# Kernel tuning notes

Measured on AMD Instinct MI355X. Metric: run time of the kernel, lower is better.

Reference implementation:

```python
import jax, jax.numpy as jnp
import numpy as np

N = 50000      # nodes
E = 800000     # directed edges (before self-loops)
IN = 128       # in_channels
H = 4          # heads (layers 1,2)
C = 64         # hidden_channels per head
OUT = 512      # out_channels of final Linear
LEAKY_SLOPE = 0.2


def _gat_layer(x, src, dst, n, W, a_src, a_dst, b, concat):
    """PyG GATConv (v1): shared linear, additive attention, segment softmax over dst."""
    heads, ch = a_src.shape
    xl = (x @ W).reshape(n, heads, ch)                       # [N,H,C]
    as_n = jnp.sum(xl * a_src, axis=-1)                      # [N,H] alpha_src per node
    ad_n = jnp.sum(xl * a_dst, axis=-1)                      # [N,H] alpha_dst per node
    logits = jax.nn.leaky_relu(as_n[src] + ad_n[dst], LEAKY_SLOPE)  # [Etot,H]
    m = jax.lax.stop_gradient(jax.ops.segment_max(logits, dst, num_segments=n))
    p = jnp.exp(logits - m[dst])
    denom = jax.ops.segment_sum(p, dst, num_segments=n) + 1e-16
    alpha = p / denom[dst]                                   # segment softmax over incoming edges
    out = jax.ops.segment_sum(xl[src] * alpha[:, :, None], dst, num_segments=n)  # [N,H,C]
    out = out.reshape(n, heads * ch) if concat else out.mean(axis=1)
    return out + b


def setup_inputs() -> dict:
    key = jax.random.key(0)
    ks = jax.random.split(key, 16)

    def gl(k, shape, fan_in):
        return jax.random.normal(k, shape, dtype=jnp.float32) * np.float32(1.0 / np.sqrt(fan_in))

    x = jax.random.normal(ks[0], (N, IN), dtype=jnp.float32)
    edge_index = jax.random.randint(ks[1], (2, E), 0, N, dtype=jnp.int32)

    inp = {
        "x": x,
        "edge_index": edge_index,
        # layer 1: in -> H*C (concat)
        "W1": gl(ks[2], (IN, H * C), IN),
        "a_src1": gl(ks[3], (H, C), C),
        "a_dst1": gl(ks[4], (H, C), C),
        "b1": jnp.zeros((H * C,), jnp.float32),
        # layer 2: H*C -> H*C (concat)
        "W2": gl(ks[5], (H * C, H * C), H * C),
        "a_src2": gl(ks[6], (H, C), C),
        "a_dst2": gl(ks[7], (H, C), C),
        "b2": jnp.zeros((H * C,), jnp.float32),
        # layer 3: H*C -> C (1 head, no concat)
        "W3": gl(ks[8], (H * C, C), H * C),
        "a_src3": gl(ks[9], (1, C), C),
        "a_dst3": gl(ks[10], (1, C), C),
        "b3": jnp.zeros((C,), jnp.float32),
        # final fc: C -> OUT
        "Wfc": gl(ks[11], (C, OUT), C),
        "bfc": jnp.zeros((OUT,), jnp.float32),
    }
    return inp


def reference(x, edge_index, W1, a_src1, a_dst1, b1, W2, a_src2, a_dst2, b2,
              W3, a_src3, a_dst3, b3, Wfc, bfc):
    n = x.shape[0]
    loop = jnp.arange(n, dtype=edge_index.dtype)             # PyG GATConv adds self-loops
    src = jnp.concatenate([edge_index[0], loop])
    dst = jnp.concatenate([edge_index[1], loop])

    h = jax.nn.relu(_gat_layer(x, src, dst, n, W1, a_src1, a_dst1, b1, True))
    h = jax.nn.relu(_gat_layer(h, src, dst, n, W2, a_src2, a_dst2, b2, True))
    h = jax.nn.relu(_gat_layer(h, src, dst, n, W3, a_src3, a_dst3, b3, False))
    return jax.nn.relu(h @ Wfc + bfc)                        # [N, OUT]
```

## Files before the change

kernel.cpp:

```cpp
#include <hip/hip_runtime.h>
#include <cstdint>
#include <cstddef>

typedef unsigned short ushort_t;
typedef __bf16 bf16x8 __attribute__((ext_vector_type(8)));
typedef float f32x4 __attribute__((ext_vector_type(4)));

__device__ __forceinline__ float b2f(ushort_t u) {
    return __uint_as_float(((unsigned int)u) << 16);
}
__device__ __forceinline__ ushort_t f2b(float f) {
    __bf16 h = (__bf16)f;
    return *(ushort_t*)&h;
}

__device__ __forceinline__ void stage8(const float* __restrict__ g, ushort_t* s) {
    float4 f0 = *(const float4*)g;
    float4 f1 = *(const float4*)(g + 4);
    union { ushort_t u[8]; uint4 v; } t;
    t.u[0] = f2b(f0.x); t.u[1] = f2b(f0.y); t.u[2] = f2b(f0.z); t.u[3] = f2b(f0.w);
    t.u[4] = f2b(f1.x); t.u[5] = f2b(f1.y); t.u[6] = f2b(f1.z); t.u[7] = f2b(f1.w);
    *(uint4*)s = t.v;
}
__device__ __forceinline__ void stage8(const ushort_t* __restrict__ g, ushort_t* s) {
    *(float4*)s = *(const float4*)g;
}

__global__ __launch_bounds__(256) void transpose_kernel(const float* __restrict__ W,
                                                        ushort_t* __restrict__ WT,
                                                        int K, int N2) {
    int id = blockIdx.x * 256 + threadIdx.x;
    if (id >= K * N2) return;
    int n = id / K, k = id - n * K;
    WT[id] = f2b(W[k * N2 + n]);
}

__global__ __launch_bounds__(256) void degree_kernel(const int* __restrict__ ei_dst,
                                                     int* __restrict__ deg, int E, int Etot) {
    int e = blockIdx.x * 256 + threadIdx.x;
    if (e >= Etot) return;
    int d = (e < E) ? ei_dst[e] : (e - E);
    atomicAdd(&deg[d], 1);
}

__global__ __launch_bounds__(1024) void scan_kernel(const int* __restrict__ deg,
                                                    int* __restrict__ rowoff, int n) {
    __shared__ int sums[1024];
    int t = threadIdx.x;
    int chunk = (n + 1023) >> 10;
    int start = t * chunk;
    int end = min(start + chunk, n);
    int s = 0;
    for (int i = start; i < end; i++) s += deg[i];
    sums[t] = s;
    __syncthreads();
    for (int off = 1; off < 1024; off <<= 1) {
        int v = (t >= off) ? sums[t - off] : 0;
        __syncthreads();
        sums[t] += v;
        __syncthreads();
    }
    int base = (t == 0) ? 0 : sums[t - 1];
    for (int i = start; i < end; i++) { rowoff[i] = base; base += deg[i]; }
    if (t == 1023) rowoff[n] = sums[1023];
}

__global__ __launch_bounds__(256) void scatter_kernel(const int* __restrict__ ei_src,
                                                      const int* __restrict__ ei_dst,
                                                      const int* __restrict__ rowoff,
                                                      int* __restrict__ cursor,
                                                      int* __restrict__ ssrc, int E, int Etot) {
    int e = blockIdx.x * 256 + threadIdx.x;
    if (e >= Etot) return;
    int s, d;
    if (e < E) { s = ei_src[e]; d = ei_dst[e]; } else { s = d = e - E; }
    int pos = rowoff[d] + atomicAdd(&cursor[d], 1);
    ssrc[pos] = s;
}

template <typename TA, bool EPI>
__global__ __launch_bounds__(256) void gemm_mfma(const TA* __restrict__ A,
                                                 const ushort_t* __restrict__ WT,
                                                 float* __restrict__ C,
                                                 ushort_t* __restrict__ Cb,
                                                 const float* __restrict__ bias,
                                                 int M, int K, int N2) {
    __shared__ ushort_t sA[64 * 32];
    __shared__ ushort_t sB[64 * 32];
    const int tid = threadIdx.x;
    const int wv = tid >> 6, lane = tid & 63;
    const int quad = lane >> 4, l16 = lane & 15;
    const int bm = blockIdx.x * 64, bn = blockIdx.y * 64;
    const int srow = tid >> 2, skof = (tid & 3) * 8;
    f32x4 acc[4] = {};

    for (int k0 = 0; k0 < K; k0 += 32) {
        int gm = bm + srow;
        gm = gm < M ? gm : M - 1;
        stage8(A + (size_t)gm * K + k0 + skof, sA + srow * 32 + skof);
        stage8(WT + (size_t)(bn + srow) * K + k0 + skof, sB + srow * 32 + skof);
        __syncthreads();

        bf16x8 af = *(const bf16x8*)(sA + (wv * 16 + l16) * 32 + quad * 8);
#pragma unroll
        for (int j = 0; j < 4; j++) {
            bf16x8 bf = *(const bf16x8*)(sB + (j * 16 + l16) * 32 + quad * 8);
            acc[j] = __builtin_amdgcn_mfma_f32_16x16x32_bf16(af, bf, acc[j], 0, 0, 0);
        }
        __syncthreads();
    }

#pragma unroll
    for (int j = 0; j < 4; j++) {
        int col = bn + j * 16 + l16;
        float bv = EPI ? bias[col] : 0.f;
#pragma unroll
        for (int r = 0; r < 4; r++) {
            int row = bm + wv * 16 + quad * 4 + r;
            if (row < M) {
                float v = acc[j][r];
                if (EPI) {
                    v += bv;
                    v = v > 0.f ? v : 0.f;
                    C[(size_t)row * N2 + col] = v;
                } else {
                    Cb[(size_t)row * N2 + col] = f2b(v);
                }
            }
        }
    }
}

template <int CH>
__global__ __launch_bounds__(256) void attn_kernel(const ushort_t* __restrict__ xl,
                                                   const float* __restrict__ a_src,
                                                   const float* __restrict__ a_dst,
                                                   float* __restrict__ as_n,
                                                   float* __restrict__ ad_n, int N) {
    int n = blockIdx.x * 4 + (threadIdx.x >> 6);
    int lane = threadIdx.x & 63;
    if (n >= N) return;
    if (CH == 256) {
        ushort4 u = ((const ushort4*)xl)[(size_t)n * 64 + lane];
        float4 av = ((const float4*)a_src)[lane];
        float4 dv = ((const float4*)a_dst)[lane];
        float x0 = b2f(u.x), x1 = b2f(u.y), x2 = b2f(u.z), x3 = b2f(u.w);
        float s = x0 * av.x + x1 * av.y + x2 * av.z + x3 * av.w;
        float d = x0 * dv.x + x1 * dv.y + x2 * dv.z + x3 * dv.w;
#pragma unroll
        for (int off = 8; off; off >>= 1) {
            s += __shfl_xor(s, off, 64);
            d += __shfl_xor(d, off, 64);
        }
        if ((lane & 15) == 0) {
            int h = lane >> 4;
            as_n[n * 4 + h] = s;
            ad_n[n * 4 + h] = d;
        }
    } else {
        float xv = b2f(xl[(size_t)n * 64 + lane]);
        float s = xv * a_src[lane];
        float d = xv * a_dst[lane];
#pragma unroll
        for (int off = 32; off; off >>= 1) {
            s += __shfl_xor(s, off, 64);
            d += __shfl_xor(d, off, 64);
        }
        if (lane == 0) { as_n[n] = s; ad_n[n] = d; }
    }
}

template <int CH>
__global__ __launch_bounds__(256) void aggregate_kernel(const ushort_t* __restrict__ xl,
                                                        const float* __restrict__ as_n,
                                                        const float* __restrict__ ad_n,
                                                        const int* __restrict__ rowoff,
                                                        const int* __restrict__ ssrc,
                                                        const float* __restrict__ bias,
                                                        ushort_t* __restrict__ hout, int N) {
    int dd = blockIdx.x * 4 + (threadIdx.x >> 6);
    int lane = threadIdx.x & 63;
    if (dd >= N) return;
    int r0 = rowoff[dd], r1 = rowoff[dd + 1];
    if (CH == 256) {
        const int h = lane >> 4;
        const float adv = ad_n[dd * 4 + h];
        const ushort4* xv = (const ushort4*)xl;
        float a0 = 0.f, a1 = 0.f, a2 = 0.f, a3 = 0.f, den = 0.f;
        int i = r0;
        for (; i + 4 <= r1; i += 4) {
            int s0 = ssrc[i], s1 = ssrc[i + 1], s2 = ssrc[i + 2], s3 = ssrc[i + 3];
            float g0 = as_n[s0 * 4 + h], g1 = as_n[s1 * 4 + h];
            float g2 = as_n[s2 * 4 + h], g3 = as_n[s3 * 4 + h];
            ushort4 u0 = xv[(size_t)s0 * 64 + lane];
            ushort4 u1 = xv[(size_t)s1 * 64 + lane];
            ushort4 u2 = xv[(size_t)s2 * 64 + lane];
            ushort4 u3 = xv[(size_t)s3 * 64 + lane];
            float l0 = g0 + adv; l0 = l0 > 0.f ? l0 : 0.2f * l0;
            float l1 = g1 + adv; l1 = l1 > 0.f ? l1 : 0.2f * l1;
            float l2 = g2 + adv; l2 = l2 > 0.f ? l2 : 0.2f * l2;
            float l3 = g3 + adv; l3 = l3 > 0.f ? l3 : 0.2f * l3;
            float p0 = __expf(l0), p1 = __expf(l1), p2 = __expf(l2), p3 = __expf(l3);
            den += p0 + p1 + p2 + p3;
            a0 += p0 * b2f(u0.x) + p1 * b2f(u1.x) + p2 * b2f(u2.x) + p3 * b2f(u3.x);
            a1 += p0 * b2f(u0.y) + p1 * b2f(u1.y) + p2 * b2f(u2.y) + p3 * b2f(u3.y);
            a2 += p0 * b2f(u0.z) + p1 * b2f(u1.z) + p2 * b2f(u2.z) + p3 * b2f(u3.z);
            a3 += p0 * b2f(u0.w) + p1 * b2f(u1.w) + p2 * b2f(u2.w) + p3 * b2f(u3.w);
        }
        for (; i < r1; i++) {
            int s = ssrc[i];
            float lg = as_n[s * 4 + h] + adv;
            lg = lg > 0.f ? lg : 0.2f * lg;
            float p = __expf(lg);
            den += p;
            ushort4 u = xv[(size_t)s * 64 + lane];
            a0 += p * b2f(u.x);
            a1 += p * b2f(u.y);
            a2 += p * b2f(u.z);
            a3 += p * b2f(u.w);
        }
        float di = 1.f / (den + 1e-16f);
        float4 bv = ((const float4*)bias)[lane];
        float v0 = a0 * di + bv.x;
        float v1 = a1 * di + bv.y;
        float v2 = a2 * di + bv.z;
        float v3 = a3 * di + bv.w;
        ushort4 o;
        o.x = f2b(v0 > 0.f ? v0 : 0.f);
        o.y = f2b(v1 > 0.f ? v1 : 0.f);
        o.z = f2b(v2 > 0.f ? v2 : 0.f);
        o.w = f2b(v3 > 0.f ? v3 : 0.f);
        ((ushort4*)hout)[(size_t)dd * 64 + lane] = o;
    } else {
        const float adv = ad_n[dd];
        float a0 = 0.f, den = 0.f;
        int i = r0;
        for (; i + 4 <= r1; i += 4) {
            int s0 = ssrc[i], s1 = ssrc[i + 1], s2 = ssrc[i + 2], s3 = ssrc[i + 3];
            float g0 = as_n[s0], g1 = as_n[s1], g2 = as_n[s2], g3 = as_n[s3];
            ushort_t u0 = xl[(size_t)s0 * 64 + lane];
            ushort_t u1 = xl[(size_t)s1 * 64 + lane];
            ushort_t u2 = xl[(size_t)s2 * 64 + lane];
            ushort_t u3 = xl[(size_t)s3 * 64 + lane];
            float l0 = g0 + adv; l0 = l0 > 0.f ? l0 : 0.2f * l0;
            float l1 = g1 + adv; l1 = l1 > 0.f ? l1 : 0.2f * l1;
            float l2 = g2 + adv; l2 = l2 > 0.f ? l2 : 0.2f * l2;
            float l3 = g3 + adv; l3 = l3 > 0.f ? l3 : 0.2f * l3;
            float p0 = __expf(l0), p1 = __expf(l1), p2 = __expf(l2), p3 = __expf(l3);
            den += p0 + p1 + p2 + p3;
            a0 += p0 * b2f(u0) + p1 * b2f(u1) + p2 * b2f(u2) + p3 * b2f(u3);
        }
        for (; i < r1; i++) {
            int s = ssrc[i];
            float lg = as_n[s] + adv;
            lg = lg > 0.f ? lg : 0.2f * lg;
            float p = __expf(lg);
            den += p;
            a0 += p * b2f(xl[(size_t)s * 64 + lane]);
        }
        float v = a0 / (den + 1e-16f) + bias[lane];
        hout[(size_t)dd * 64 + lane] = f2b(v > 0.f ? v : 0.f);
    }
}

extern "C" void kernel_launch(void* const* d_in, const int* in_sizes, int n_in,
                              void* d_out, int out_size, void* d_ws, size_t ws_size,
                              hipStream_t stream) {
    const int N = in_sizes[0] / 128;
    const int E = in_sizes[1] / 2;
    const int Etot = E + N;

    const float* x = (const float*)d_in[0];
    const int* ei = (const int*)d_in[1];
    const int* ei_src = ei;
    const int* ei_dst = ei + E;
    float* out = (float*)d_out;

    const float* as1 = (const float*)d_in[3];
    const float* ad1 = (const float*)d_in[4];
    const float* b1  = (const float*)d_in[5];
    const float* as2 = (const float*)d_in[7];
    const float* ad2 = (const float*)d_in[8];
    const float* b2  = (const float*)d_in[9];
    const float* as3 = (const float*)d_in[11];
    const float* ad3 = (const float*)d_in[12];
    const float* b3  = (const float*)d_in[13];
    const float* bfc = (const float*)d_in[15];

    ushort_t* bufX = (ushort_t*)d_ws;
    ushort_t* bufH = bufX + (size_t)N * 256;
    ushort_t* W1T  = bufH + (size_t)N * 256;
    ushort_t* W2T  = W1T + 32768;
    ushort_t* W3T  = W2T + 65536;
    ushort_t* WfcT = W3T + 16384;
    float* asn = (float*)(WfcT + 32768);
    float* adn = asn + (size_t)N * 4;
    int* deg    = (int*)(adn + (size_t)N * 4);
    int* rowoff = deg + N;
    int* cursor = rowoff + N + 1;
    int* ssrc   = cursor + N;

    transpose_kernel<<<(128 * 256 + 255) / 256, 256, 0, stream>>>((const float*)d_in[2], W1T, 128, 256);
    transpose_kernel<<<(256 * 256 + 255) / 256, 256, 0, stream>>>((const float*)d_in[6], W2T, 256, 256);
    transpose_kernel<<<(256 * 64 + 255) / 256, 256, 0, stream>>>((const float*)d_in[10], W3T, 256, 64);
    transpose_kernel<<<(64 * 512 + 255) / 256, 256, 0, stream>>>((const float*)d_in[14], WfcT, 64, 512);

    hipMemsetAsync(deg, 0, (size_t)(3 * N + 1) * sizeof(int), stream);
    int eb = (Etot + 255) / 256;
    degree_kernel<<<eb, 256, 0, stream>>>(ei_dst, deg, E, Etot);
    scan_kernel<<<1, 1024, 0, stream>>>(deg, rowoff, N);
    scatter_kernel<<<eb, 256, 0, stream>>>(ei_src, ei_dst, rowoff, cursor, ssrc, E, Etot);

    const int MB = (N + 63) / 64;
    int nb4 = (N + 3) / 4;

    gemm_mfma<float, false><<<dim3(MB, 4), 256, 0, stream>>>(x, W1T, nullptr, bufX, nullptr, N, 128, 256);
    attn_kernel<256><<<nb4, 256, 0, stream>>>(bufX, as1, ad1, asn, adn, N);
    aggregate_kernel<256><<<nb4, 256, 0, stream>>>(bufX, asn, adn, rowoff, ssrc, b1, bufH, N);

    gemm_mfma<ushort_t, false><<<dim3(MB, 4), 256, 0, stream>>>(bufH, W2T, nullptr, bufX, nullptr, N, 256, 256);
    attn_kernel<256><<<nb4, 256, 0, stream>>>(bufX, as2, ad2, asn, adn, N);
    aggregate_kernel<256><<<nb4, 256, 0, stream>>>(bufX, asn, adn, rowoff, ssrc, b2, bufH, N);

    gemm_mfma<ushort_t, false><<<dim3(MB, 1), 256, 0, stream>>>(bufH, W3T, nullptr, bufX, nullptr, N, 256, 64);
    attn_kernel<64><<<nb4, 256, 0, stream>>>(bufX, as3, ad3, asn, adn, N);
    aggregate_kernel<64><<<nb4, 256, 0, stream>>>(bufX, asn, adn, rowoff, ssrc, b3, bufH, N);

    gemm_mfma<ushort_t, true><<<dim3(MB, 8), 256, 0, stream>>>(bufH, WfcT, out, nullptr, bfc, N, 64, 512);
}
```

Baseline: 573.7 us.

## Replace single-block prefix scan with three-pass multi-block scan

Replaces the single 1024-thread block that serially scanned the node degrees with a reduce-then-scan scheme: per-block partial sums, a one-block scan of the block sums, then a per-block scan that adds the offsets. The old kernel ran on one CU with strided, uncoalesced serial loops of about 49 elements per thread. The new version spreads the work across about 196 blocks with coalesced access, at the cost of two extra kernel launches. It assumes at most 256 blocks, so N can be at most 65536.

```diff
diff --git a/kernel.cpp b/kernel.cpp
--- a/kernel.cpp
+++ b/kernel.cpp
@@ -43,26 +43,56 @@
     atomicAdd(&deg[d], 1);
 }
 
-__global__ __launch_bounds__(1024) void scan_kernel(const int* __restrict__ deg,
-                                                    int* __restrict__ rowoff, int n) {
-    __shared__ int sums[1024];
+__global__ __launch_bounds__(256) void partial_sum_kernel(const int* __restrict__ deg,
+                                                          int* __restrict__ bsum, int n) {
+    __shared__ int ws[4];
     int t = threadIdx.x;
-    int chunk = (n + 1023) >> 10;
-    int start = t * chunk;
-    int end = min(start + chunk, n);
-    int s = 0;
-    for (int i = start; i < end; i++) s += deg[i];
-    sums[t] = s;
+    int i = blockIdx.x * 256 + t;
+    int v = (i < n) ? deg[i] : 0;
+#pragma unroll
+    for (int off = 32; off; off >>= 1) v += __shfl_xor(v, off, 64);
+    if ((t & 63) == 0) ws[t >> 6] = v;
     __syncthreads();
-    for (int off = 1; off < 1024; off <<= 1) {
-        int v = (t >= off) ? sums[t - off] : 0;
-        __syncthreads();
-        sums[t] += v;
-        __syncthreads();
-    }
-    int base = (t == 0) ? 0 : sums[t - 1];
-    for (int i = start; i < end; i++) { rowoff[i] = base; base += deg[i]; }
-    if (t == 1023) rowoff[n] = sums[1023];
+    if (t == 0) bsum[blockIdx.x] = ws[0] + ws[1] + ws[2] + ws[3];
+}
+
+__global__ __launch_bounds__(256) void scan_bsum_kernel(const int* __restrict__ bsum,
+                                                        int* __restrict__ boff,
+                                                        int* __restrict__ rowoff,
+                                                        int nblk, int n) {
+    __shared__ int sm[256];
+    int t = threadIdx.x;
+    int v = (t < nblk) ? bsum[t] : 0;
+    sm[t] = v;
+    __syncthreads();
+#pragma unroll
+    for (int off = 1; off < 256; off <<= 1) {
+        int u = (t >= off) ? sm[t - off] : 0;
+        __syncthreads();
+        sm[t] += u;
+        __syncthreads();
+    }
+    if (t < nblk) boff[t] = sm[t] - v;
+    if (t == 255) rowoff[n] = sm[255];
+}
+
+__global__ __launch_bounds__(256) void block_scan_kernel(const int* __restrict__ deg,
+                                                         const int* __restrict__ boff,
+                                                         int* __restrict__ rowoff, int n) {
+    __shared__ int sm[256];
+    int t = threadIdx.x;
+    int i = blockIdx.x * 256 + t;
+    int v = (i < n) ? deg[i] : 0;
+    sm[t] = v;
+    __syncthreads();
+#pragma unroll
+    for (int off = 1; off < 256; off <<= 1) {
+        int u = (t >= off) ? sm[t - off] : 0;
+        __syncthreads();
+        sm[t] += u;
+        __syncthreads();
+    }
+    if (i < n) rowoff[i] = boff[blockIdx.x] + sm[t] - v;
 }
 
 __global__ __launch_bounds__(256) void scatter_kernel(const int* __restrict__ ei_src,
@@ -299,6 +329,8 @@
     int* rowoff = deg + N;
     int* cursor = rowoff + N + 1;
     int* ssrc   = cursor + N;
+    int* bsum   = ssrc + Etot;
+    int* boff   = bsum + 256;
 
     transpose_kernel<<<(128 * 256 + 255) / 256, 256, 0, stream>>>((const float*)d_in[2], W1T, 128, 256);
     transpose_kernel<<<(256 * 256 + 255) / 256, 256, 0, stream>>>((const float*)d_in[6], W2T, 256, 256);
@@ -308,7 +340,10 @@
     hipMemsetAsync(deg, 0, (size_t)(3 * N + 1) * sizeof(int), stream);
     int eb = (Etot + 255) / 256;
     degree_kernel<<<eb, 256, 0, stream>>>(ei_dst, deg, E, Etot);
-    scan_kernel<<<1, 1024, 0, stream>>>(deg, rowoff, N);
+    const int NBLK = (N + 255) / 256;
+    partial_sum_kernel<<<NBLK, 256, 0, stream>>>(deg, bsum, N);
+    scan_bsum_kernel<<<1, 256, 0, stream>>>(bsum, boff, rowoff, NBLK, N);
+    block_scan_kernel<<<NBLK, 256, 0, stream>>>(deg, boff, rowoff, N);
     scatter_kernel<<<eb, 256, 0, stream>>>(ei_src, ei_dst, rowoff, cursor, ssrc, E, Etot);
 
     const int MB = (N + 63) / 64;
```

After: 511.1 us. 10.9% less time.
